# Performance work log

Measured on AMD Instinct MI355X. Metric: run time of the kernel, lower is better.

Reference implementation:

```python
import jax, jax.numpy as jnp
import numpy as np

NUM_HEADS = 4
HEAD_K = 256
HEAD_V = 512
CHUNK = 64
GATE_NORMALIZER = 16.0
EPS = 1e-5


def _gla_chunk(q, k, v, gk):
    """Chunked gated linear attention.
    q,k,gk: [B,H,S,Dk]; v: [B,H,S,Dv]. gk is log-decay (<=0).
    Recurrence: S_t = diag(exp(gk_t)) S_{t-1} + k_t v_t^T ; o_t = scale * q_t S_t.
    """
    B, H, S, Dk = q.shape
    Dv = v.shape[-1]
    N = S // CHUNK
    scale = Dk ** -0.5

    def to_chunks(x):
        # [B,H,S,D] -> [N,B,H,C,D]
        return x.reshape(B, H, N, CHUNK, x.shape[-1]).transpose(2, 0, 1, 3, 4)

    qc, kc, vc, gkc = map(to_chunks, (q, k, v, gk))
    gc = jnp.cumsum(gkc, axis=-2)  # inclusive cumulative log-decay within chunk

    tri = jnp.tril(jnp.ones((CHUNK, CHUNK), dtype=q.dtype))  # causal incl. diagonal

    def step(Sstate, xs):
        qi, ki, vi, gi = xs  # [B,H,C,Dk]/[B,H,C,Dv]
        q_g = qi * jnp.exp(gi) * scale            # [B,H,C,Dk]
        k_g = ki * jnp.exp(-gi)                   # [B,H,C,Dk]
        A = jnp.einsum('bhid,bhjd->bhij', q_g, k_g) * tri
        o_intra = jnp.einsum('bhij,bhjе->bhiе'.replace('е', 'e'), A, vi)
        o_inter = jnp.einsum('bhcd,bhde->bhce', q_g, Sstate)
        g_last = gi[:, :, -1, :]                  # [B,H,Dk]
        k_dec = ki * jnp.exp(g_last[:, :, None, :] - gi)
        S_new = Sstate * jnp.exp(g_last)[..., None] + jnp.einsum('bhcd,bhce->bhde', k_dec, vi)
        return S_new, o_intra + o_inter

    S0 = jnp.zeros((B, H, Dk, Dv), dtype=q.dtype)
    _, o = jax.lax.scan(step, S0, (qc, kc, vc, gc))
    # [N,B,H,C,Dv] -> [B,H,S,Dv]
    return o.transpose(1, 2, 0, 3, 4).reshape(B, H, S, Dv)


def setup_inputs() -> dict:
    key = jax.random.key(0)
    ks = jax.random.split(key, 10)
    B, S, Hd = 2, 2048, 2048
    key_dim = NUM_HEADS * HEAD_K   # 1024
    value_dim = NUM_HEADS * HEAD_V  # 2048
    lr = 16  # gate_low_rank_dim
    w = lambda k, shp: (jax.random.normal(k, shp, dtype=jnp.float32) * 0.02)
    return {
        'hidden_states': jax.random.normal(ks[0], (B, S, Hd), dtype=jnp.float32),
        'Wq': w(ks[1], (Hd, key_dim)),
        'Wk': w(ks[2], (Hd, key_dim)),
        'Wv': w(ks[3], (Hd, value_dim)),
        'Wgk1': w(ks[4], (Hd, lr)),
        'Wgk2': w(ks[5], (lr, key_dim)),
        'bgk2': jnp.zeros((key_dim,), dtype=jnp.float32),
        'Wg': w(ks[6], (Hd, value_dim)),
        'g_norm_weight': jnp.ones((HEAD_V,), dtype=jnp.float32),
        'Wo': w(ks[7], (value_dim, Hd)),
    }


def reference(hidden_states, Wq, Wk, Wv, Wgk1, Wgk2, bgk2, Wg, g_norm_weight, Wo):
    B, S, Hd = hidden_states.shape
    x = hidden_states
    # projections
    q = (x @ Wq).reshape(B, S, NUM_HEADS, HEAD_K).transpose(0, 2, 1, 3)
    k = (x @ Wk).reshape(B, S, NUM_HEADS, HEAD_K).transpose(0, 2, 1, 3)
    v = (x @ Wv).reshape(B, S, NUM_HEADS, HEAD_V).transpose(0, 2, 1, 3)
    gk = (x @ Wgk1) @ Wgk2 + bgk2
    gk = jax.nn.log_sigmoid(gk) / GATE_NORMALIZER
    gk = gk.reshape(B, S, NUM_HEADS, HEAD_K).transpose(0, 2, 1, 3)

    o = _gla_chunk(q, k, v, gk)  # [B,H,S,Dv]
    o = o.transpose(0, 2, 1, 3)  # [B,S,H,Dv]

    # fused RMSNorm + swish gate
    g = (x @ Wg).reshape(B, S, NUM_HEADS, HEAD_V)
    rms = jnp.sqrt(jnp.mean(o * o, axis=-1, keepdims=True) + EPS)
    o = (o / rms) * g_norm_weight * (g * jax.nn.sigmoid(g))
    o = o.reshape(B, S, NUM_HEADS * HEAD_V)
    return o @ Wo
```

## Files before the change

kernel.cpp:

```cpp
#include <hip/hip_runtime.h>
#include <hip/hip_bf16.h>

#define B_   2
#define S_   2048
#define HD_  2048
#define H_   4
#define DK_  256
#define DV_  512
#define KD_  1024
#define VD_  2048
#define ND_  6144
#define M_   4096
#define NCHUNK_ 32
#define CHUNK_  64

typedef __attribute__((ext_vector_type(8))) short bf16x8;
typedef __attribute__((ext_vector_type(4))) float f32x4;
typedef __attribute__((ext_vector_type(4))) unsigned short us4;
typedef __attribute__((ext_vector_type(8))) unsigned short us8;

__device__ __forceinline__ unsigned short f2bf(float f) {
    __hip_bfloat16 h = __float2bfloat16(f);
    return *reinterpret_cast<unsigned short*>(&h);
}
__device__ __forceinline__ float bf2f(unsigned short u) {
    unsigned int x = ((unsigned int)u) << 16;
    return *reinterpret_cast<float*>(&x);
}

__global__ __launch_bounds__(256) void conv_bf16(const float* __restrict__ in,
                                                 unsigned short* __restrict__ out) {
    const int idx = blockIdx.x * 256 + threadIdx.x;
    float4 a = *(const float4*)&in[(size_t)idx * 4];
    us4 w; w.x = f2bf(a.x); w.y = f2bf(a.y); w.z = f2bf(a.z); w.w = f2bf(a.w);
    *(us4*)&out[(size_t)idx * 4] = w;
}

__global__ __launch_bounds__(256) void tr_w(const float* __restrict__ W,
                                            unsigned short* __restrict__ Wt,
                                            int K, int N) {
    __shared__ float Ws[32][33];
    const int t = threadIdx.x;
    const int n0 = blockIdx.x * 32, k0 = blockIdx.y * 32;
    const int r = t >> 3, c4 = (t & 7) * 4;
    float4 a = *(const float4*)&W[(size_t)(k0 + r) * N + n0 + c4];
    Ws[r][c4 + 0] = a.x; Ws[r][c4 + 1] = a.y; Ws[r][c4 + 2] = a.z; Ws[r][c4 + 3] = a.w;
    __syncthreads();
    const int nr = t >> 3, kc4 = (t & 7) * 4;
    us4 w;
#pragma unroll
    for (int j = 0; j < 4; ++j) w[j] = f2bf(Ws[kc4 + j][nr]);
    *(us4*)&Wt[(size_t)(n0 + nr) * K + k0 + kc4] = w;
}

__global__ __launch_bounds__(256) void tr_v(const unsigned short* __restrict__ qkvg,
                                            unsigned short* __restrict__ vT) {
    __shared__ unsigned short Ws[32][36];
    const int t = threadIdx.x;
    const int c0 = blockIdx.x * 32;
    const int s0 = blockIdx.y * 32;
    {
        const int r = t >> 3, c4 = (t & 7) * 4;
        us4 w = *(const us4*)&qkvg[(size_t)(s0 + r) * ND_ + 2048 + c0 + c4];
        *(us4*)&Ws[r][c4] = w;
    }
    __syncthreads();
    const int er = t >> 3, sc4 = (t & 7) * 4;
    const int c = c0 + er;
    const int h = c >> 9, e = c & 511;
    const int b = s0 >> 11, srow = s0 & 2047;
    us4 w;
#pragma unroll
    for (int j = 0; j < 4; ++j) w[j] = Ws[sc4 + j][er];
    *(us4*)&vT[((size_t)(b * H_ + h) * 512 + e) * 2048 + srow + sc4] = w;
}

__global__ __launch_bounds__(256) void gemm_bt(const unsigned short* __restrict__ A,
                                               const unsigned short* __restrict__ Bt,
                                               float* __restrict__ Cf,
                                               unsigned short* __restrict__ Cb,
                                               int M, int N, int K) {
    __shared__ __align__(16) unsigned short As[128 * 32];
    __shared__ __align__(16) unsigned short Bs[128 * 32];
    const int t = threadIdx.x;
    const int m0 = blockIdx.y * 128, n0 = blockIdx.x * 128;
    const int wave = t >> 6, lane = t & 63;
    const int quad = lane >> 4, l16 = lane & 15;
    const int wm = (wave >> 1) * 64, wn = (wave & 1) * 64;
    const int srow = t >> 2, scol = (t & 3) * 8;

    f32x4 acc[4][4] = {};

    us8 a0 = *(const us8*)&A[(size_t)(m0 + srow) * K + scol];
    us8 a1 = *(const us8*)&A[(size_t)(m0 + srow + 64) * K + scol];
    us8 b0 = *(const us8*)&Bt[(size_t)(n0 + srow) * K + scol];
    us8 b1 = *(const us8*)&Bt[(size_t)(n0 + srow + 64) * K + scol];

    for (int k0 = 0; k0 < K; k0 += 32) {
        __syncthreads();
        *(us8*)&As[srow * 32 + scol] = a0;
        *(us8*)&As[(srow + 64) * 32 + scol] = a1;
        *(us8*)&Bs[srow * 32 + scol] = b0;
        *(us8*)&Bs[(srow + 64) * 32 + scol] = b1;
        __syncthreads();
        if (k0 + 32 < K) {
            a0 = *(const us8*)&A[(size_t)(m0 + srow) * K + k0 + 32 + scol];
            a1 = *(const us8*)&A[(size_t)(m0 + srow + 64) * K + k0 + 32 + scol];
            b0 = *(const us8*)&Bt[(size_t)(n0 + srow) * K + k0 + 32 + scol];
            b1 = *(const us8*)&Bt[(size_t)(n0 + srow + 64) * K + k0 + 32 + scol];
        }

        bf16x8 af[4], bfr[4];
#pragma unroll
        for (int i = 0; i < 4; ++i)
            af[i] = *(const bf16x8*)&As[(wm + i * 16 + l16) * 32 + quad * 8];
#pragma unroll
        for (int j = 0; j < 4; ++j)
            bfr[j] = *(const bf16x8*)&Bs[(wn + j * 16 + l16) * 32 + quad * 8];
#pragma unroll
        for (int i = 0; i < 4; ++i)
#pragma unroll
            for (int j = 0; j < 4; ++j)
                acc[i][j] = __builtin_amdgcn_mfma_f32_16x16x32_bf16(af[i], bfr[j], acc[i][j], 0, 0, 0);
    }

    if (Cb) {
#pragma unroll
        for (int i = 0; i < 4; ++i)
#pragma unroll
            for (int j = 0; j < 4; ++j)
#pragma unroll
                for (int r = 0; r < 4; ++r)
                    Cb[(size_t)(m0 + wm + i * 16 + quad * 4 + r) * N + n0 + wn + j * 16 + l16] = f2bf(acc[i][j][r]);
    } else {
#pragma unroll
        for (int i = 0; i < 4; ++i)
#pragma unroll
            for (int j = 0; j < 4; ++j)
#pragma unroll
                for (int r = 0; r < 4; ++r)
                    Cf[(size_t)(m0 + wm + i * 16 + quad * 4 + r) * N + n0 + wn + j * 16 + l16] = acc[i][j][r];
    }
}

__global__ __launch_bounds__(256) void gemm_n16(const float* __restrict__ X,
                                                const float* __restrict__ W,
                                                float* __restrict__ T) {
    __shared__ float Xs[16][129];
    __shared__ float Wsh[128][17];
    const int t = threadIdx.x;
    const int m0 = blockIdx.x * 16;
    const int mm = t >> 4, jj = t & 15;
    float acc = 0.f;
    for (int k0 = 0; k0 < HD_; k0 += 128) {
        __syncthreads();
#pragma unroll
        for (int p = 0; p < 2; ++p) {
            int q = t + p * 256;
            int r = q >> 5, c4 = (q & 31) * 4;
            float4 a = *(const float4*)&X[(size_t)(m0 + r) * HD_ + k0 + c4];
            Xs[r][c4 + 0] = a.x; Xs[r][c4 + 1] = a.y; Xs[r][c4 + 2] = a.z; Xs[r][c4 + 3] = a.w;
        }
#pragma unroll
        for (int p = 0; p < 8; ++p) {
            int q = t + p * 256;
            int r = q >> 4, c = q & 15;
            Wsh[r][c] = W[(size_t)(k0 + r) * 16 + c];
        }
        __syncthreads();
#pragma unroll 16
        for (int kk = 0; kk < 128; ++kk) acc += Xs[mm][kk] * Wsh[kk][jj];
    }
    T[(size_t)(m0 + mm) * 16 + jj] = acc;
}

__global__ __launch_bounds__(256) void gk_act(const float* __restrict__ T,
                                              const float* __restrict__ W2,
                                              const float* __restrict__ b2,
                                              float* __restrict__ gk) {
    const int idx = blockIdx.x * 256 + threadIdx.x;
    const int n = idx & 1023;
    const int m = idx >> 10;
    float acc = b2[n];
#pragma unroll
    for (int j = 0; j < 16; ++j) acc += T[m * 16 + j] * W2[j * 1024 + n];
    float ls = (acc < 0.f) ? (acc - log1pf(expf(acc))) : (-log1pf(expf(-acc)));
    gk[idx] = ls * 0.0625f;
}

__global__ __launch_bounds__(256) void gate_prep(const unsigned short* __restrict__ qkvg,
                                                 const float* __restrict__ gk,
                                                 unsigned short* __restrict__ qg,
                                                 unsigned short* __restrict__ kg,
                                                 unsigned short* __restrict__ kgT,
                                                 float* __restrict__ glexp) {
    const int idx = blockIdx.x * 256 + threadIdx.x;
    const int d = idx & 255;
    const int chunk = (idx >> 8) & 31;
    const int h = (idx >> 13) & 3;
    const int b = idx >> 15;
    const int bh = b * H_ + h;
    const size_t col = h * 256 + d;
    const size_t rowbase = (size_t)b * S_ + chunk * 64;
    const size_t kgT_base = ((size_t)bh * 256 + d) * 2048 + chunk * 64;
    const float scale = 0.0625f;
    float gc = 0.f;
    for (int t = 0; t < 64; ++t) {
        size_t r = rowbase + t;
        gc += gk[r * (size_t)KD_ + col];
        unsigned short qv = qkvg[r * (size_t)ND_ + col];
        unsigned short kv = qkvg[r * (size_t)ND_ + 1024 + col];
        unsigned short kgv = f2bf(bf2f(kv) * expf(-gc));
        qg[r * (size_t)KD_ + col] = f2bf(bf2f(qv) * expf(gc) * scale);
        kg[r * (size_t)KD_ + col] = kgv;
        kgT[kgT_base + t] = kgv;
    }
    glexp[idx] = expf(gc);
}

__global__ __launch_bounds__(256) void pass_c1(const unsigned short* __restrict__ qg,
                                               const unsigned short* __restrict__ kg,
                                               unsigned short* __restrict__ Asg) {
    __shared__ __align__(16) unsigned short Aq[64 * 32];
    __shared__ __align__(16) unsigned short Bk[64 * 32];
    const int t = threadIdx.x;
    const int bhc = blockIdx.x;
    const int chunk = bhc & 31, bh = bhc >> 5;
    const int h = bh & 3, b = bh >> 2;
    const int s0 = chunk * 64;
    const int wave = t >> 6, lane = t & 63;
    const int quad = lane >> 4, l16 = lane & 15;
    const int srow = t >> 2, scol = (t & 3) * 8;
    const size_t base = (size_t)b * S_ * KD_ + h * DK_ + (size_t)(s0 + srow) * KD_ + scol;

    f32x4 acc[4] = {};
    us8 aq = *(const us8*)&qg[base];
    us8 bk = *(const us8*)&kg[base];

    for (int k0 = 0; k0 < 256; k0 += 32) {
        __syncthreads();
        *(us8*)&Aq[srow * 32 + scol] = aq;
        *(us8*)&Bk[srow * 32 + scol] = bk;
        __syncthreads();
        if (k0 + 32 < 256) {
            aq = *(const us8*)&qg[base + k0 + 32];
            bk = *(const us8*)&kg[base + k0 + 32];
        }
        bf16x8 bfr = *(const bf16x8*)&Bk[(wave * 16 + l16) * 32 + quad * 8];
#pragma unroll
        for (int i = 0; i < 4; ++i) {
            bf16x8 af = *(const bf16x8*)&Aq[(i * 16 + l16) * 32 + quad * 8];
            acc[i] = __builtin_amdgcn_mfma_f32_16x16x32_bf16(af, bfr, acc[i], 0, 0, 0);
        }
    }

    const int j = wave * 16 + l16;
#pragma unroll
    for (int i = 0; i < 4; ++i)
#pragma unroll
        for (int r = 0; r < 4; ++r) {
            int m = i * 16 + quad * 4 + r;
            float val = (j <= m) ? acc[i][r] : 0.f;
            Asg[(size_t)bhc * 4096 + m * 64 + j] = f2bf(val);
        }
}

__global__ __launch_bounds__(256) void pass_a(const unsigned short* __restrict__ kgT,
                                              const unsigned short* __restrict__ vT,
                                              unsigned short* __restrict__ Dt) {
    __shared__ __align__(16) unsigned short As[128 * 32];
    __shared__ __align__(16) unsigned short Bs[128 * 32];
    const int t = threadIdx.x;
    const int bhc = blockIdx.z;
    const int chunk = bhc & 31, bh = bhc >> 5;
    const int s0 = chunk * 64;
    const int e0 = blockIdx.y * 128;
    const int d0 = blockIdx.x * 128;
    const int wave = t >> 6, lane = t & 63;
    const int quad = lane >> 4, l16 = lane & 15;
    const int wm = (wave >> 1) * 64, wn = (wave & 1) * 64;

    f32x4 acc[4][4] = {};

    for (int k0 = 0; k0 < 64; k0 += 32) {
        __syncthreads();
#pragma unroll
        for (int p = 0; p < 2; ++p) {
            int q = t + p * 256;
            int row = q >> 2, c8 = (q & 3) * 8;
            us8 wv = *(const us8*)&vT[((size_t)bh * 512 + e0 + row) * 2048 + s0 + k0 + c8];
            *(us8*)&As[row * 32 + c8] = wv;
            us8 wk = *(const us8*)&kgT[((size_t)bh * 256 + d0 + row) * 2048 + s0 + k0 + c8];
            *(us8*)&Bs[row * 32 + c8] = wk;
        }
        __syncthreads();

        bf16x8 af[4], bfr[4];
#pragma unroll
        for (int i = 0; i < 4; ++i)
            af[i] = *(const bf16x8*)&As[(wm + i * 16 + l16) * 32 + quad * 8];
#pragma unroll
        for (int j = 0; j < 4; ++j)
            bfr[j] = *(const bf16x8*)&Bs[(wn + j * 16 + l16) * 32 + quad * 8];
#pragma unroll
        for (int i = 0; i < 4; ++i)
#pragma unroll
            for (int j = 0; j < 4; ++j)
                acc[i][j] = __builtin_amdgcn_mfma_f32_16x16x32_bf16(af[i], bfr[j], acc[i][j], 0, 0, 0);
    }

#pragma unroll
    for (int i = 0; i < 4; ++i)
#pragma unroll
        for (int j = 0; j < 4; ++j)
#pragma unroll
            for (int r = 0; r < 4; ++r) {
                size_t e = e0 + wm + i * 16 + quad * 4 + r;
                size_t d = d0 + wn + j * 16 + l16;
                Dt[((size_t)bhc * 512 + e) * 256 + d] = f2bf(acc[i][j][r]);
            }
}

__global__ __launch_bounds__(256) void pass_b(unsigned short* __restrict__ DtSt,
                                              const float* __restrict__ gle) {
    const int gid = blockIdx.x * 256 + threadIdx.x;
    const int bh = gid >> 14;
    const int rem = gid & 16383;
    const int e = rem >> 5;
    const int d8 = (rem & 31) * 8;

    float S[8];
#pragma unroll
    for (int i = 0; i < 8; ++i) S[i] = 0.f;

    for (int n = 0; n < NCHUNK_; ++n) {
        const size_t row = (((size_t)(bh * 32 + n)) * 512 + e) * 256 + d8;
        us8 dv = *(const us8*)&DtSt[row];
        us8 w;
#pragma unroll
        for (int i = 0; i < 8; ++i) w[i] = f2bf(S[i]);
        *(us8*)&DtSt[row] = w;
        float4 e0 = *(const float4*)&gle[(size_t)(bh * 32 + n) * 256 + d8];
        float4 e1 = *(const float4*)&gle[(size_t)(bh * 32 + n) * 256 + d8 + 4];
        float E[8] = {e0.x, e0.y, e0.z, e0.w, e1.x, e1.y, e1.z, e1.w};
#pragma unroll
        for (int i = 0; i < 8; ++i) S[i] = (S[i] + bf2f(dv[i])) * E[i];
    }
}

__global__ __launch_bounds__(256) void pass_c2(const unsigned short* __restrict__ qg,
                                               const unsigned short* __restrict__ vT,
                                               const unsigned short* __restrict__ Asg,
                                               const unsigned short* __restrict__ St,
                                               unsigned short* __restrict__ o) {
    __shared__ __align__(16) unsigned short At[64 * 32];
    __shared__ __align__(16) unsigned short Bt[256 * 32];
    const int t = threadIdx.x;
    const int bhc = blockIdx.z;
    const int chunk = bhc & 31, bh = bhc >> 5;
    const int h = bh & 3, b = bh >> 2;
    const int s0 = chunk * 64;
    const int eh = blockIdx.x * 256;
    const int wave = t >> 6, lane = t & 63;
    const int quad = lane >> 4, l16 = lane & 15;
    const int we = wave * 64;

    f32x4 acc[4][4] = {};

    for (int kk0 = 0; kk0 < 10; ++kk0) {
        __syncthreads();
        if (kk0 < 2) {
            {
                int row = t >> 2, c8 = (t & 3) * 8;
                us8 w = *(const us8*)&Asg[(size_t)bhc * 4096 + row * 64 + kk0 * 32 + c8];
                *(us8*)&At[row * 32 + c8] = w;
            }
            const int t0 = kk0 * 32;
#pragma unroll
            for (int p = 0; p < 4; ++p) {
                int q = t + p * 256;
                int row = q >> 2, c8 = (q & 3) * 8;
                us8 w = *(const us8*)&vT[((size_t)bh * 512 + eh + row) * 2048 + s0 + t0 + c8];
                *(us8*)&Bt[row * 32 + c8] = w;
            }
        } else {
            const int d0 = (kk0 - 2) * 32;
            {
                int row = t >> 2, c8 = (t & 3) * 8;
                us8 w = *(const us8*)&qg[((size_t)b * S_ + s0 + row) * KD_ + h * DK_ + d0 + c8];
                *(us8*)&At[row * 32 + c8] = w;
            }
#pragma unroll
            for (int p = 0; p < 4; ++p) {
                int q = t + p * 256;
                int row = q >> 2, c8 = (q & 3) * 8;
                us8 w = *(const us8*)&St[(((size_t)bhc) * 512 + eh + row) * 256 + d0 + c8];
                *(us8*)&Bt[row * 32 + c8] = w;
            }
        }
        __syncthreads();

        bf16x8 af[4], bfr[4];
#pragma unroll
        for (int i = 0; i < 4; ++i)
            af[i] = *(const bf16x8*)&At[(i * 16 + l16) * 32 + quad * 8];
#pragma unroll
        for (int j = 0; j < 4; ++j)
            bfr[j] = *(const bf16x8*)&Bt[(we + j * 16 + l16) * 32 + quad * 8];
#pragma unroll
        for (int i = 0; i < 4; ++i)
#pragma unroll
            for (int j = 0; j < 4; ++j)
                acc[i][j] = __builtin_amdgcn_mfma_f32_16x16x32_bf16(af[i], bfr[j], acc[i][j], 0, 0, 0);
    }

#pragma unroll
    for (int i = 0; i < 4; ++i)
#pragma unroll
        for (int j = 0; j < 4; ++j)
#pragma unroll
            for (int r = 0; r < 4; ++r) {
                int m = i * 16 + quad * 4 + r;
                int e = eh + we + j * 16 + l16;
                o[((size_t)b * S_ + s0 + m) * VD_ + h * DV_ + e] = f2bf(acc[i][j][r]);
            }
}

__global__ __launch_bounds__(256) void postnorm(const unsigned short* __restrict__ o,
                                                const unsigned short* __restrict__ qkvg,
                                                const float* __restrict__ gnw,
                                                unsigned short* __restrict__ obf) {
    const int row = blockIdx.x;
    const int wave = threadIdx.x >> 6;
    const int lane = threadIdx.x & 63;
    const size_t base = (size_t)row * VD_ + wave * 512;
    const size_t gbase = (size_t)row * ND_ + 4096 + wave * 512;
    float x[8];
    float ss = 0.f;
#pragma unroll
    for (int j = 0; j < 8; ++j) {
        x[j] = bf2f(o[base + lane + j * 64]);
        ss += x[j] * x[j];
    }
#pragma unroll
    for (int off = 32; off; off >>= 1) ss += __shfl_xor(ss, off);
    const float inv = 1.0f / sqrtf(ss * (1.0f / 512.0f) + 1e-5f);
#pragma unroll
    for (int j = 0; j < 8; ++j) {
        int e = lane + j * 64;
        float gv = bf2f(qkvg[gbase + e]);
        float sig = 1.0f / (1.0f + expf(-gv));
        obf[base + e] = f2bf(x[j] * inv * gnw[e] * (gv * sig));
    }
}

extern "C" void kernel_launch(void* const* d_in, const int* in_sizes, int n_in,
                              void* d_out, int out_size, void* d_ws, size_t ws_size,
                              hipStream_t stream) {
    const float* x    = (const float*)d_in[0];
    const float* Wq   = (const float*)d_in[1];
    const float* Wk   = (const float*)d_in[2];
    const float* Wv   = (const float*)d_in[3];
    const float* Wgk1 = (const float*)d_in[4];
    const float* Wgk2 = (const float*)d_in[5];
    const float* bgk2 = (const float*)d_in[6];
    const float* Wg   = (const float*)d_in[7];
    const float* gnw  = (const float*)d_in[8];
    const float* Wo   = (const float*)d_in[9];
    float* out = (float*)d_out;

    float* ws = (float*)d_ws;
    const size_t MF = 1048576;
    typedef unsigned short us;
    us* WotT   = (us*)(ws);
    us* qkvg   = (us*)(ws + 2 * MF);
    us* qg     = (us*)(ws + 15 * MF);
    us* kg     = (us*)(ws + 17 * MF);
    us* kgT    = (us*)(ws + 19 * MF);
    us* vT     = (us*)(ws + 21 * MF);
    float* T   = ws + 25 * MF;
    float* gle = T + 65536;
    us* Asg    = (us*)(ws + 25 * MF + 131072);
    us* DtSt   = (us*)(ws + 25 * MF + 786432);
    us* xb     = (us*)(ws + 41 * MF + 786432);
    float* gkb = ws + 41 * MF + 786432;
    us* WcatT  = (us*)(ws + 45 * MF + 786432);
    us* o      = (us*)(ws + 45 * MF + 786432);
    us* obf    = (us*)(ws + 49 * MF + 786432);

    dim3 blk(256);
    conv_bf16<<<8192, blk, 0, stream>>>(x, xb);
    tr_w<<<dim3(32, 64), blk, 0, stream>>>(Wq, WcatT,                   HD_, KD_);
    tr_w<<<dim3(32, 64), blk, 0, stream>>>(Wk, WcatT + 1024 * 2048,     HD_, KD_);
    tr_w<<<dim3(64, 64), blk, 0, stream>>>(Wv, WcatT + 2048 * 2048,     HD_, VD_);
    tr_w<<<dim3(64, 64), blk, 0, stream>>>(Wg, WcatT + (size_t)4096 * 2048, HD_, VD_);
    tr_w<<<dim3(64, 64), blk, 0, stream>>>(Wo, WotT, VD_, HD_);

    gemm_bt<<<dim3(48, 32), blk, 0, stream>>>(xb, WcatT, nullptr, qkvg, M_, ND_, HD_);
    tr_v<<<dim3(64, 128), blk, 0, stream>>>(qkvg, vT);

    gemm_n16<<<M_ / 16, blk, 0, stream>>>(x, Wgk1, T);
    gk_act<<<(M_ * KD_) / 256, blk, 0, stream>>>(T, Wgk2, bgk2, gkb);
    gate_prep<<<(B_ * H_ * NCHUNK_ * DK_) / 256, blk, 0, stream>>>(qkvg, gkb, qg, kg, kgT, gle);

    pass_c1<<<256, blk, 0, stream>>>(qg, kg, Asg);
    pass_a<<<dim3(2, 4, 256), blk, 0, stream>>>(kgT, vT, DtSt);
    pass_b<<<512, blk, 0, stream>>>(DtSt, gle);
    pass_c2<<<dim3(2, 1, 256), blk, 0, stream>>>(qg, vT, Asg, DtSt, o);
    postnorm<<<M_, blk, 0, stream>>>(o, qkvg, gnw, obf);
    gemm_bt<<<dim3(16, 32), blk, 0, stream>>>(obf, WotT, out, nullptr, M_, HD_, VD_);
}
```

Measured before the change: 500.8 us.

## Use direct global-to-LDS loads in GEMM and chunk kernels

Replaces register-staged global loads followed by LDS stores with the global_load_lds builtin, which writes 16 bytes per lane directly into shared memory, across the main GEMM and three chunk-attention kernels. This removes the VGPR staging and separate ds_write instructions. It also drops the software prefetch of the next K tile, so loads are no longer overlapped with the previous iteration's MFMAs and each iteration now waits for its own loads. Correctness relies on wave-contiguous LDS placement matching the previous row/column layout, and on the compiler inserting the vmcnt wait before the barrier.

```diff
diff --git a/kernel.cpp b/kernel.cpp
--- a/kernel.cpp
+++ b/kernel.cpp
@@ -28,6 +28,12 @@
     return *reinterpret_cast<float*>(&x);
 }
 
+typedef const __attribute__((address_space(1))) unsigned int* gas_ptr;
+typedef __attribute__((address_space(3))) unsigned int* las_ptr;
+__device__ __forceinline__ void gload16(const void* g, void* l) {
+    __builtin_amdgcn_global_load_lds((gas_ptr)g, (las_ptr)l, 16, 0, 0);
+}
+
 __global__ __launch_bounds__(256) void conv_bf16(const float* __restrict__ in,
                                                  unsigned short* __restrict__ out) {
     const int idx = blockIdx.x * 256 + threadIdx.x;
@@ -91,24 +97,22 @@
 
     f32x4 acc[4][4] = {};
 
-    us8 a0 = *(const us8*)&A[(size_t)(m0 + srow) * K + scol];
-    us8 a1 = *(const us8*)&A[(size_t)(m0 + srow + 64) * K + scol];
-    us8 b0 = *(const us8*)&Bt[(size_t)(n0 + srow) * K + scol];
-    us8 b1 = *(const us8*)&Bt[(size_t)(n0 + srow + 64) * K + scol];
+    const unsigned short* Ar0 = &A[(size_t)(m0 + srow) * K + scol];
+    const unsigned short* Ar1 = &A[(size_t)(m0 + srow + 64) * K + scol];
+    const unsigned short* Br0 = &Bt[(size_t)(n0 + srow) * K + scol];
+    const unsigned short* Br1 = &Bt[(size_t)(n0 + srow + 64) * K + scol];
+    unsigned short* lA0 = &As[wave * 512];
+    unsigned short* lA1 = &As[2048 + wave * 512];
+    unsigned short* lB0 = &Bs[wave * 512];
+    unsigned short* lB1 = &Bs[2048 + wave * 512];
 
     for (int k0 = 0; k0 < K; k0 += 32) {
         __syncthreads();
-        *(us8*)&As[srow * 32 + scol] = a0;
-        *(us8*)&As[(srow + 64) * 32 + scol] = a1;
-        *(us8*)&Bs[srow * 32 + scol] = b0;
-        *(us8*)&Bs[(srow + 64) * 32 + scol] = b1;
-        __syncthreads();
-        if (k0 + 32 < K) {
-            a0 = *(const us8*)&A[(size_t)(m0 + srow) * K + k0 + 32 + scol];
-            a1 = *(const us8*)&A[(size_t)(m0 + srow + 64) * K + k0 + 32 + scol];
-            b0 = *(const us8*)&Bt[(size_t)(n0 + srow) * K + k0 + 32 + scol];
-            b1 = *(const us8*)&Bt[(size_t)(n0 + srow + 64) * K + k0 + 32 + scol];
-        }
+        gload16(Ar0 + k0, lA0);
+        gload16(Ar1 + k0, lA1);
+        gload16(Br0 + k0, lB0);
+        gload16(Br1 + k0, lB1);
+        __syncthreads();
 
         bf16x8 af[4], bfr[4];
 #pragma unroll
@@ -234,18 +238,14 @@
     const size_t base = (size_t)b * S_ * KD_ + h * DK_ + (size_t)(s0 + srow) * KD_ + scol;
 
     f32x4 acc[4] = {};
-    us8 aq = *(const us8*)&qg[base];
-    us8 bk = *(const us8*)&kg[base];
+    unsigned short* lA = &Aq[wave * 512];
+    unsigned short* lB = &Bk[wave * 512];
 
     for (int k0 = 0; k0 < 256; k0 += 32) {
         __syncthreads();
-        *(us8*)&Aq[srow * 32 + scol] = aq;
-        *(us8*)&Bk[srow * 32 + scol] = bk;
-        __syncthreads();
-        if (k0 + 32 < 256) {
-            aq = *(const us8*)&qg[base + k0 + 32];
-            bk = *(const us8*)&kg[base + k0 + 32];
-        }
+        gload16(&qg[base + k0], lA);
+        gload16(&kg[base + k0], lB);
+        __syncthreads();
         bf16x8 bfr = *(const bf16x8*)&Bk[(wave * 16 + l16) * 32 + quad * 8];
 #pragma unroll
         for (int i = 0; i < 4; ++i) {
@@ -288,10 +288,10 @@
         for (int p = 0; p < 2; ++p) {
             int q = t + p * 256;
             int row = q >> 2, c8 = (q & 3) * 8;
-            us8 wv = *(const us8*)&vT[((size_t)bh * 512 + e0 + row) * 2048 + s0 + k0 + c8];
-            *(us8*)&As[row * 32 + c8] = wv;
-            us8 wk = *(const us8*)&kgT[((size_t)bh * 256 + d0 + row) * 2048 + s0 + k0 + c8];
-            *(us8*)&Bs[row * 32 + c8] = wk;
+            gload16(&vT[((size_t)bh * 512 + e0 + row) * 2048 + s0 + k0 + c8],
+                    &As[p * 2048 + wave * 512]);
+            gload16(&kgT[((size_t)bh * 256 + d0 + row) * 2048 + s0 + k0 + c8],
+                    &Bs[p * 2048 + wave * 512]);
         }
         __syncthreads();
 
@@ -366,36 +366,31 @@
     const int we = wave * 64;
 
     f32x4 acc[4][4] = {};
+    const int srow = t >> 2, scol = (t & 3) * 8;
 
     for (int kk0 = 0; kk0 < 10; ++kk0) {
         __syncthreads();
         if (kk0 < 2) {
-            {
-                int row = t >> 2, c8 = (t & 3) * 8;
-                us8 w = *(const us8*)&Asg[(size_t)bhc * 4096 + row * 64 + kk0 * 32 + c8];
-                *(us8*)&At[row * 32 + c8] = w;
-            }
+            gload16(&Asg[(size_t)bhc * 4096 + srow * 64 + kk0 * 32 + scol],
+                    &At[wave * 512]);
             const int t0 = kk0 * 32;
 #pragma unroll
             for (int p = 0; p < 4; ++p) {
                 int q = t + p * 256;
                 int row = q >> 2, c8 = (q & 3) * 8;
-                us8 w = *(const us8*)&vT[((size_t)bh * 512 + eh + row) * 2048 + s0 + t0 + c8];
-                *(us8*)&Bt[row * 32 + c8] = w;
+                gload16(&vT[((size_t)bh * 512 + eh + row) * 2048 + s0 + t0 + c8],
+                        &Bt[p * 2048 + wave * 512]);
             }
         } else {
             const int d0 = (kk0 - 2) * 32;
-            {
-                int row = t >> 2, c8 = (t & 3) * 8;
-                us8 w = *(const us8*)&qg[((size_t)b * S_ + s0 + row) * KD_ + h * DK_ + d0 + c8];
-                *(us8*)&At[row * 32 + c8] = w;
-            }
+            gload16(&qg[((size_t)b * S_ + s0 + srow) * KD_ + h * DK_ + d0 + scol],
+                    &At[wave * 512]);
 #pragma unroll
             for (int p = 0; p < 4; ++p) {
                 int q = t + p * 256;
                 int row = q >> 2, c8 = (q & 3) * 8;
-                us8 w = *(const us8*)&St[(((size_t)bhc) * 512 + eh + row) * 256 + d0 + c8];
-                *(us8*)&Bt[row * 32 + c8] = w;
+                gload16(&St[(((size_t)bhc) * 512 + eh + row) * 256 + d0 + c8],
+                        &Bt[p * 2048 + wave * 512]);
             }
         }
         __syncthreads();
```

Measured after the change: 537.5 us. 7.3% more time.
